# Optimization experiments

Hardware: AMD Instinct MI355X
Metric: run time of the kernel (lower is better)

The kernel has to match this reference:

```python
import jax, jax.numpy as jnp
import numpy as np
from jax import lax

B, CIN, H, W = 8, 256, 32, 32
DK, DV, NH = 256, 256, 8
DKH = DK // NH
COUT = 512  # output_dim; conv path has COUT - DV channels
KS, PAD = 3, 1


def setup_inputs() -> dict:
    key = jax.random.key(0)
    ks = jax.random.split(key, 9)
    scale = DKH ** (-0.5)
    return {
        "x": jax.random.normal(ks[0], (B, CIN, H, W), jnp.float32),
        "w_qkv": jax.random.normal(ks[1], (2 * DK + DV, CIN), jnp.float32) * 0.02,
        "b_qkv": jnp.zeros((2 * DK + DV,), jnp.float32),
        "w_attn": jax.random.normal(ks[2], (DV, DV), jnp.float32) * 0.02,
        "b_attn": jnp.zeros((DV,), jnp.float32),
        "w_out": jax.random.normal(ks[3], (COUT - DV, CIN, KS, KS), jnp.float32) * 0.02,
        "b_out": jnp.zeros((COUT - DV,), jnp.float32),
        # original: dkh**-0.5 + torch.rand(2*W-1, dkh)
        "key_rel_w": scale + jax.random.uniform(ks[4], (2 * W - 1, DKH), jnp.float32),
        "key_rel_h": scale + jax.random.uniform(ks[5], (2 * H - 1, DKH), jnp.float32),
    }


def _conv1x1(x, w, b):
    return jnp.einsum("bchw,oc->bohw", x, w) + b[None, :, None, None]


def _rel_to_abs(x):
    # x: [b, nh, L, 2L-1] -> [b, nh, L, L] via pad-reshape-slice trick
    b, nh, L, _ = x.shape
    x = jnp.pad(x, ((0, 0), (0, 0), (0, 0), (0, 1)))            # [b,nh,L,2L]
    flat = x.reshape(b, nh, L * 2 * L)
    flat = jnp.pad(flat, ((0, 0), (0, 0), (0, L - 1)))
    final = flat.reshape(b, nh, L + 1, 2 * L - 1)
    return final[:, :, :L, L - 1:]


def _rel_logits_1d(q5, rel_k, h, w, nh, perm):
    # q5: [b, nh, dkh, h, w]; rel_k: [2w-1, dkh]
    b = q5.shape[0]
    rel = jnp.einsum("bhdxy,md->bhxym", q5, rel_k)               # [b,nh,h,w,2w-1]
    rel = rel.reshape(b, nh * h, w, 2 * w - 1)
    rel = _rel_to_abs(rel)                                        # [b,nh*h,w,w]
    rel = rel.reshape(b, nh, h, w, w)
    rel = jnp.broadcast_to(rel[:, :, :, None], (b, nh, h, h, w, w))
    rel = jnp.transpose(rel, perm)                                # [b,nh,H,W,H,W]
    return rel.reshape(b, nh, h * w, h * w)


def reference(x, w_qkv, b_qkv, w_attn, b_attn, w_out, b_out, key_rel_w, key_rel_h):
    b = x.shape[0]
    hw = H * W
    # parallel conv path (3x3, pad 1)
    conv_out = lax.conv_general_dilated(
        x, w_out, window_strides=(1, 1), padding=((PAD, PAD), (PAD, PAD)),
        dimension_numbers=("NCHW", "OIHW", "NCHW")) + b_out[None, :, None, None]
    # qkv via 1x1 conv
    qkv = _conv1x1(x, w_qkv, b_qkv)
    q, k, v = jnp.split(qkv, [DK, 2 * DK], axis=1)
    q = q.reshape(b, NH, DKH, hw) * (DKH ** (-0.5))
    k = k.reshape(b, NH, DKH, hw)
    v = v.reshape(b, NH, DV // NH, hw)
    logits = jnp.einsum("bhdq,bhdk->bhqk", q, k)                  # [b,nh,HW,HW]
    q5 = q.reshape(b, NH, DKH, H, W)
    w_rel = _rel_logits_1d(q5, key_rel_w, H, W, NH, (0, 1, 2, 4, 3, 5))
    h_rel = _rel_logits_1d(jnp.transpose(q5, (0, 1, 2, 4, 3)), key_rel_h, W, H, NH,
                           (0, 1, 4, 2, 5, 3))
    logits = logits + h_rel + w_rel
    weights = jax.nn.softmax(logits, axis=-1)
    attn = jnp.einsum("bhqk,bhdk->bhdq", weights, v)              # [b,nh,dvh,HW]
    attn = attn.reshape(b, DV, H, W)
    attn = _conv1x1(attn, w_attn, b_attn)
    return jnp.concatenate([conv_out, attn], axis=1)
```

## Files before the change

kernel.cpp:

```cpp
#include <hip/hip_runtime.h>
#include <hip/hip_bf16.h>


typedef __hip_bfloat16 bf16;
using short8 = __attribute__((ext_vector_type(8))) short;
using short4v = __attribute__((ext_vector_type(4))) short;
using f32x4 = __attribute__((ext_vector_type(4))) float;

__device__ __forceinline__ short f2bs(float f) {
  union { bf16 b; short s; } u; u.b = __float2bfloat16(f); return u.s;
}
__device__ __forceinline__ float bs2f(short s) {
  union { unsigned u; float f; } x; x.u = ((unsigned)(unsigned short)s) << 16;
  return x.f;
}

__global__ __launch_bounds__(256) void xpose(
    const float* __restrict__ X, short* __restrict__ xt,
    short* __restrict__ xb2) {
  const int b = blockIdx.x, r = blockIdx.y;
  const int tid = threadIdx.x;
  if (r == 0 || r == 33) {
    short8 z = {};
    short* dst = xt + (((size_t)b * 34 + r) * 34) * 256;
    for (int g = tid; g < 1088; g += 256) *(short8*)(dst + g * 8) = z;
    return;
  }
  __shared__ short xls[32][264];
  {
    const float* src = X + (size_t)b * 256 * 1024 + (r - 1) * 32;
    for (int it = 0; it < 8; ++it) {
      int idx = it * 256 + tid;
      int c = idx >> 3, pq = idx & 7;
      float4 f4 = *(const float4*)(src + (size_t)c * 1024 + pq * 4);
      xls[pq * 4 + 0][c] = f2bs(f4.x);
      xls[pq * 4 + 1][c] = f2bs(f4.y);
      xls[pq * 4 + 2][c] = f2bs(f4.z);
      xls[pq * 4 + 3][c] = f2bs(f4.w);
    }
  }
  __syncthreads();
  {
    short* dst = xt + (((size_t)b * 34 + r) * 34) * 256;
    for (int it = 0; it < 4; ++it) {
      int idx = it * 256 + tid;
      int cc = idx >> 5, co = idx & 31;
      short8 v = *(const short8*)&xls[cc][co * 8];
      *(short8*)(dst + (cc + 1) * 256 + co * 8) = v;
    }
    if (tid < 64) {
      short8 z = {};
      int cce = (tid >> 5) * 33, co = tid & 31;
      *(short8*)(dst + cce * 256 + co * 8) = z;
    }
  }
  {
    short* dst = xb2 + (((size_t)b * 64 + (r - 1) * 2) * 8) * 512;
    for (int it = 0; it < 4; ++it) {
      int g = it * 256 + tid;
      int half = g >> 9, c8 = (g >> 6) & 7, grp = (g >> 4) & 3, pcol = g & 15;
      short8 v = *(const short8*)&xls[half * 16 + pcol][c8 * 32 + grp * 8];
      *(short8*)(dst + ((half * 8 + c8) * 64 + grp * 16 + pcol) * 8) = v;
    }
  }
}

__global__ __launch_bounds__(256) void wpack(
    const float* __restrict__ Wc, short* __restrict__ Wb,
    const float* __restrict__ wq, short* __restrict__ Wq,
    const float* __restrict__ wa, short* __restrict__ Wa) {
  const int bid = blockIdx.x;
  const int tid = threadIdx.x;
  if (bid < 256) {
    __shared__ float ws[2304];
    const float* src = Wc + (size_t)bid * 2304;
    for (int it = 0; it < 9; ++it) ws[it * 256 + tid] = src[it * 256 + tid];
    __syncthreads();
#pragma unroll
    for (int tap = 0; tap < 9; ++tap)
      Wb[tap * 65536 + bid * 256 + tid] = f2bs(ws[tid * 9 + tap]);
  } else if (bid < 1024) {
    int idx = (bid - 256) * 256 + tid;
    Wq[idx] = f2bs(wq[idx]);
  } else {
    int idx = (bid - 1024) * 256 + tid;
    Wa[idx] = f2bs(wa[idx]);
  }
}

__global__ __launch_bounds__(256) void qkv_mfma(
    const short* __restrict__ Wq, const short* __restrict__ xb2,
    const float* __restrict__ bias,
    short* __restrict__ qsb, short* __restrict__ ksb, short* __restrict__ vtb) {
  const int tid = threadIdx.x;
  const int w = tid >> 6, lane = tid & 63;
  const int col = lane & 15, grp = lane >> 4, g8 = grp * 8;
  const int b = blockIdx.z;
  const int p0 = blockIdx.x * 64;
  const int og = blockIdx.y * 128;
  const int ob = og + w * 16;

  const short* wa0 = Wq + (size_t)(ob + col) * 256 + g8;
  const short* wa1 = wa0 + (size_t)64 * 256;
  const short* xpb = xb2 + (((size_t)b * 64 + blockIdx.x * 4) * 8) * 512 + lane * 8;

  f32x4 acc[2][4] = {};
#pragma unroll
  for (int c8 = 0; c8 < 8; ++c8) {
    const int chb = c8 * 32;
    short8 a0 = *(const short8*)(wa0 + chb);
    short8 a1 = *(const short8*)(wa1 + chb);
    short8 b0 = *(const short8*)(xpb + c8 * 512);
    short8 b1 = *(const short8*)(xpb + 4096 + c8 * 512);
    short8 b2 = *(const short8*)(xpb + 8192 + c8 * 512);
    short8 b3 = *(const short8*)(xpb + 12288 + c8 * 512);
    acc[0][0] = __builtin_amdgcn_mfma_f32_16x16x32_bf16(a0, b0, acc[0][0], 0, 0, 0);
    acc[0][1] = __builtin_amdgcn_mfma_f32_16x16x32_bf16(a0, b1, acc[0][1], 0, 0, 0);
    acc[0][2] = __builtin_amdgcn_mfma_f32_16x16x32_bf16(a0, b2, acc[0][2], 0, 0, 0);
    acc[0][3] = __builtin_amdgcn_mfma_f32_16x16x32_bf16(a0, b3, acc[0][3], 0, 0, 0);
    acc[1][0] = __builtin_amdgcn_mfma_f32_16x16x32_bf16(a1, b0, acc[1][0], 0, 0, 0);
    acc[1][1] = __builtin_amdgcn_mfma_f32_16x16x32_bf16(a1, b1, acc[1][1], 0, 0, 0);
    acc[1][2] = __builtin_amdgcn_mfma_f32_16x16x32_bf16(a1, b2, acc[1][2], 0, 0, 0);
    acc[1][3] = __builtin_amdgcn_mfma_f32_16x16x32_bf16(a1, b3, acc[1][3], 0, 0, 0);
  }

  const float qscale = 0.17677669529663687f;
#pragma unroll
  for (int j = 0; j < 2; ++j) {
    const int obase = ob + j * 64 + grp * 4;
    const int sect = obase >> 8;
    const int nh = (obase >> 5) & 7;
    const int d0 = obase & 31;
    const size_t hb = ((size_t)(b * 8 + nh)) * 1024;
    float bv[4];
#pragma unroll
    for (int r = 0; r < 4; ++r) bv[r] = bias[obase + r];
    if (sect == 0) {
#pragma unroll
      for (int pp = 0; pp < 4; ++pp) {
        const int p = p0 + pp * 16 + col;
        short4v o4;
#pragma unroll
        for (int r = 0; r < 4; ++r)
          o4[r] = f2bs((acc[j][pp][r] + bv[r]) * qscale);
        *(short4v*)&qsb[(hb + p) * 32 + d0] = o4;
      }
    } else if (sect == 1) {
#pragma unroll
      for (int pp = 0; pp < 4; ++pp) {
        const int p = p0 + pp * 16 + col;
        short4v o4;
#pragma unroll
        for (int r = 0; r < 4; ++r)
          o4[r] = f2bs(acc[j][pp][r] + bv[r]);
        *(short4v*)&ksb[(hb + p) * 32 + d0] = o4;
      }
    } else {
#pragma unroll
      for (int pp = 0; pp < 4; ++pp) {
        const int p = p0 + pp * 16 + col;
#pragma unroll
        for (int r = 0; r < 4; ++r)
          vtb[hb * 32 + (size_t)(d0 + r) * 1024 + p] = f2bs(acc[j][pp][r] + bv[r]);
      }
    }
  }
}

__global__ __launch_bounds__(256, 4) void attn_mfma(
    const short* __restrict__ qsb, const short* __restrict__ ksb,
    const short* __restrict__ vtb,
    const float* __restrict__ relw_g, const float* __restrict__ relh_g,
    short* __restrict__ amt) {
  const int tid = threadIdx.x;
  const int w = tid >> 6, lane = tid & 63;
  const int col = lane & 15, grp = lane >> 4, g8 = grp * 8;
  const int qt = blockIdx.x * 4 + w;
  const int bnh = blockIdx.y;
  const int q0 = qt * 16;
  const int i = qt >> 1;
  const int j0 = (qt & 1) * 16;

  const short* Qb = qsb + (size_t)bnh * 32768;
  const short* Kb = ksb + (size_t)bnh * 32768;
  const short* Vb = vtb + (size_t)bnh * 32768;

  __shared__ short Gh_s[4][16][68];
  __shared__ short kvb[2][8][512];
  __shared__ short Pt_s[4][2][16][40];
  short* Gw_w = &Pt_s[w][0][0][0];

  const short* gK = Kb + (size_t)(w * 16 + col) * 32 + g8;
  const short* gV = Vb + (size_t)((w & 1) * 16 + col) * 1024 + (w >> 1) * 32 + g8;

  short8 stgK = *(const short8*)gK;
  short8 stgV = *(const short8*)gV;

  short8 b_q = *(const short8*)(Qb + (q0 + col) * 32 + g8);

  {
    const float* rels[2] = {relh_g, relw_g};
#pragma unroll
    for (int tb = 0; tb < 2; ++tb) {
      const float* relg = rels[tb];
#pragma unroll
      for (int t = 0; t < 4; ++t) {
        int m = 16 * t + col;
        int mc = m > 62 ? 62 : m;
        const float* rp = relg + mc * 32 + g8;
        float4 f0 = *(const float4*)rp;
        float4 f1 = *(const float4*)(rp + 4);
        short8 ar;
        ar[0] = f2bs(f0.x); ar[1] = f2bs(f0.y);
        ar[2] = f2bs(f0.z); ar[3] = f2bs(f0.w);
        ar[4] = f2bs(f1.x); ar[5] = f2bs(f1.y);
        ar[6] = f2bs(f1.z); ar[7] = f2bs(f1.w);
        f32x4 d = __builtin_amdgcn_mfma_f32_16x16x32_bf16(
            ar, b_q, (f32x4){0.f, 0.f, 0.f, 0.f}, 0, 0, 0);
        short4v o;
        o[0] = f2bs(d[0]); o[1] = f2bs(d[1]);
        o[2] = f2bs(d[2]); o[3] = f2bs(d[3]);
        short* Gd = tb ? Gw_w : &Gh_s[w][0][0];
        *(short4v*)(Gd + col * 68 + 16 * t + grp * 4) = o;
      }
    }
  }
  __asm__ volatile("s_waitcnt lgkmcnt(0)" ::: "memory");

  float gw[8];
#pragma unroll
  for (int t = 0; t < 2; ++t)
#pragma unroll
    for (int r = 0; r < 4; ++r)
      gw[t * 4 + r] =
          bs2f(Gw_w[col * 68 + t * 16 + grp * 4 + r - j0 - col + 31]);

  const short8 a_one = {0x3F80, 0x3F80, 0x3F80, 0x3F80,
                        0x3F80, 0x3F80, 0x3F80, 0x3F80};

  f32x4 acc0 = {0.f, 0.f, 0.f, 0.f};
  f32x4 acc1 = {0.f, 0.f, 0.f, 0.f};
  f32x4 accl = {0.f, 0.f, 0.f, 0.f};

  short8 cvA0p = {}, cvA1p = {}, cvB0p = {}, cvB1p = {};

  *(short8*)&kvb[0][w][lane * 8] = stgK;
  *(short8*)&kvb[0][4 + w][lane * 8] = stgV;
  __syncthreads();

#pragma unroll 2
  for (int it = 0; it < 16; ++it) {
    const int cur = it & 1;
    if (it < 15) {
      stgK = *(const short8*)(gK + (size_t)(it + 1) * 2048);
      stgV = *(const short8*)(gV + (size_t)(it + 1) * 64);
    }
    short8 ck0  = *(const short8*)&kvb[cur][0][lane * 8];
    short8 ck1  = *(const short8*)&kvb[cur][1][lane * 8];
    short8 ck2  = *(const short8*)&kvb[cur][2][lane * 8];
    short8 ck3  = *(const short8*)&kvb[cur][3][lane * 8];
    short8 cva0 = *(const short8*)&kvb[cur][4][lane * 8];
    short8 cva1 = *(const short8*)&kvb[cur][5][lane * 8];
    short8 cvb0 = *(const short8*)&kvb[cur][6][lane * 8];
    short8 cvb1 = *(const short8*)&kvb[cur][7][lane * 8];

    f32x4 s0 = __builtin_amdgcn_mfma_f32_16x16x32_bf16(
        ck0, b_q, (f32x4){0.f, 0.f, 0.f, 0.f}, 0, 0, 0);
    f32x4 s1 = __builtin_amdgcn_mfma_f32_16x16x32_bf16(
        ck1, b_q, (f32x4){0.f, 0.f, 0.f, 0.f}, 0, 0, 0);
    f32x4 s2 = __builtin_amdgcn_mfma_f32_16x16x32_bf16(
        ck2, b_q, (f32x4){0.f, 0.f, 0.f, 0.f}, 0, 0, 0);
    f32x4 s3 = __builtin_amdgcn_mfma_f32_16x16x32_bf16(
        ck3, b_q, (f32x4){0.f, 0.f, 0.f, 0.f}, 0, 0, 0);

    if (it > 0) {
      short8 pA = *(const short8*)&Pt_s[w][0][col][g8];
      short8 pB = *(const short8*)&Pt_s[w][1][col][g8];
      acc0 = __builtin_amdgcn_mfma_f32_16x16x32_bf16(cvA0p, pA, acc0, 0, 0, 0);
      acc0 = __builtin_amdgcn_mfma_f32_16x16x32_bf16(cvB0p, pB, acc0, 0, 0, 0);
      acc1 = __builtin_amdgcn_mfma_f32_16x16x32_bf16(cvA1p, pA, acc1, 0, 0, 0);
      acc1 = __builtin_amdgcn_mfma_f32_16x16x32_bf16(cvB1p, pB, acc1, 0, 0, 0);
      accl = __builtin_amdgcn_mfma_f32_16x16x32_bf16(a_one, pA, accl, 0, 0, 0);
      accl = __builtin_amdgcn_mfma_f32_16x16x32_bf16(a_one, pB, accl, 0, 0, 0);
    }

    float ghA = bs2f(Gh_s[w][col][2 * it - i + 31]);
    float ghB = bs2f(Gh_s[w][col][2 * it + 1 - i + 31]);
    short4v p0, p1, p2, p3;
#pragma unroll
    for (int r = 0; r < 4; ++r) p0[r] = f2bs(__expf(s0[r] + ghA + gw[r]));
#pragma unroll
    for (int r = 0; r < 4; ++r) p1[r] = f2bs(__expf(s1[r] + ghA + gw[4 + r]));
#pragma unroll
    for (int r = 0; r < 4; ++r) p2[r] = f2bs(__expf(s2[r] + ghB + gw[r]));
#pragma unroll
    for (int r = 0; r < 4; ++r) p3[r] = f2bs(__expf(s3[r] + ghB + gw[4 + r]));
    *(short4v*)&Pt_s[w][0][col][grp * 4] = p0;
    *(short4v*)&Pt_s[w][0][col][16 + grp * 4] = p1;
    *(short4v*)&Pt_s[w][1][col][grp * 4] = p2;
    *(short4v*)&Pt_s[w][1][col][16 + grp * 4] = p3;

    if (it < 15) {
      *(short8*)&kvb[cur ^ 1][w][lane * 8] = stgK;
      *(short8*)&kvb[cur ^ 1][4 + w][lane * 8] = stgV;
    }
    cvA0p = cva0; cvA1p = cva1; cvB0p = cvb0; cvB1p = cvb1;
    __syncthreads();
  }

  {
    short8 pA = *(const short8*)&Pt_s[w][0][col][g8];
    short8 pB = *(const short8*)&Pt_s[w][1][col][g8];
    acc0 = __builtin_amdgcn_mfma_f32_16x16x32_bf16(cvA0p, pA, acc0, 0, 0, 0);
    acc0 = __builtin_amdgcn_mfma_f32_16x16x32_bf16(cvB0p, pB, acc0, 0, 0, 0);
    acc1 = __builtin_amdgcn_mfma_f32_16x16x32_bf16(cvA1p, pA, acc1, 0, 0, 0);
    acc1 = __builtin_amdgcn_mfma_f32_16x16x32_bf16(cvB1p, pB, acc1, 0, 0, 0);
    accl = __builtin_amdgcn_mfma_f32_16x16x32_bf16(a_one, pA, accl, 0, 0, 0);
    accl = __builtin_amdgcn_mfma_f32_16x16x32_bf16(a_one, pB, accl, 0, 0, 0);
  }

  float rn = 1.0f / accl[0];
  const int bq = bnh >> 3, nh = bnh & 7;
  short* amb = amt + ((size_t)bq * 1024 + q0 + col) * 256 + nh * 32;
  short4v o4a, o4b;
#pragma unroll
  for (int r = 0; r < 4; ++r) {
    o4a[r] = f2bs(acc0[r] * rn);
    o4b[r] = f2bs(acc1[r] * rn);
  }
  *(short4v*)&amb[grp * 4] = o4a;
  *(short4v*)&amb[16 + grp * 4] = o4b;
}

__global__ __launch_bounds__(256) void proj_mfma(
    const short* __restrict__ Wa, const short* __restrict__ amt,
    const float* __restrict__ bias, float* __restrict__ out) {
  const int tid = threadIdx.x;
  const int w = tid >> 6, lane = tid & 63;
  const int col = lane & 15, grp = lane >> 4, g8 = grp * 8;
  const int b = blockIdx.z;
  const int p0 = blockIdx.x * 64;
  const int og = blockIdx.y * 128;
  const int ob = og + w * 16;

  const short* wa0 = Wa + (size_t)(ob + col) * 256 + g8;
  const short* wa1 = wa0 + (size_t)64 * 256;
  const short* xp0 = amt + ((size_t)b * 1024 + p0 + col) * 256 + g8;
  const short* xp1 = xp0 + (size_t)16 * 256;
  const short* xp2 = xp0 + (size_t)32 * 256;
  const short* xp3 = xp0 + (size_t)48 * 256;

  f32x4 acc[2][4] = {};
#pragma unroll
  for (int c8 = 0; c8 < 8; ++c8) {
    const int chb = c8 * 32;
    short8 a0 = *(const short8*)(wa0 + chb);
    short8 a1 = *(const short8*)(wa1 + chb);
    short8 b0 = *(const short8*)(xp0 + chb);
    short8 b1 = *(const short8*)(xp1 + chb);
    short8 b2 = *(const short8*)(xp2 + chb);
    short8 b3 = *(const short8*)(xp3 + chb);
    acc[0][0] = __builtin_amdgcn_mfma_f32_16x16x32_bf16(a0, b0, acc[0][0], 0, 0, 0);
    acc[0][1] = __builtin_amdgcn_mfma_f32_16x16x32_bf16(a0, b1, acc[0][1], 0, 0, 0);
    acc[0][2] = __builtin_amdgcn_mfma_f32_16x16x32_bf16(a0, b2, acc[0][2], 0, 0, 0);
    acc[0][3] = __builtin_amdgcn_mfma_f32_16x16x32_bf16(a0, b3, acc[0][3], 0, 0, 0);
    acc[1][0] = __builtin_amdgcn_mfma_f32_16x16x32_bf16(a1, b0, acc[1][0], 0, 0, 0);
    acc[1][1] = __builtin_amdgcn_mfma_f32_16x16x32_bf16(a1, b1, acc[1][1], 0, 0, 0);
    acc[1][2] = __builtin_amdgcn_mfma_f32_16x16x32_bf16(a1, b2, acc[1][2], 0, 0, 0);
    acc[1][3] = __builtin_amdgcn_mfma_f32_16x16x32_bf16(a1, b3, acc[1][3], 0, 0, 0);
  }

#pragma unroll
  for (int j = 0; j < 2; ++j) {
    const int obase = ob + j * 64 + grp * 4;
    float bv[4];
#pragma unroll
    for (int r = 0; r < 4; ++r) bv[r] = bias[obase + r];
#pragma unroll
    for (int pp = 0; pp < 4; ++pp) {
      const int p = p0 + pp * 16 + col;
#pragma unroll
      for (int r = 0; r < 4; ++r)
        out[((size_t)b * 512 + 256 + obase + r) * 1024 + p] =
            acc[j][pp][r] + bv[r];
    }
  }
}

__global__ __launch_bounds__(256) void conv_mfma(
    const short* __restrict__ xt, const short* __restrict__ Wb,
    const float* __restrict__ bias, float* __restrict__ out) {
  const int tid = threadIdx.x;
  const int w = tid >> 6, lane = tid & 63;
  const int col = lane & 15, grp = lane >> 4, g8 = grp * 8;
  const int r0 = blockIdx.x;
  const int oh = blockIdx.y;
  const int bb = blockIdx.z;

  __shared__ short xs[3][34][264];

  {
    const short* src = xt + (((size_t)bb * 34 + r0) * 34) * 256;
    for (int g = tid; g < 3264; g += 256) {
      int row = g / 1088;
      int rem = g - row * 1088;
      int cc = rem >> 5, chg = rem & 31;
      short8 v = *(const short8*)(src + (row * 34 + cc) * 256 + chg * 8);
      *(short8*)&xs[row][cc][chg * 8] = v;
    }
  }
  __syncthreads();

  const int ob0 = oh * 128 + w * 16;
  const int ob1 = ob0 + 64;
  const short* Wa0 = Wb + (ob0 + col) * 256 + g8;
  const short* Wa1 = Wb + (ob1 + col) * 256 + g8;

  f32x4 acc00 = {0.f, 0.f, 0.f, 0.f};
  f32x4 acc01 = {0.f, 0.f, 0.f, 0.f};
  f32x4 acc10 = {0.f, 0.f, 0.f, 0.f};
  f32x4 acc11 = {0.f, 0.f, 0.f, 0.f};

#pragma unroll 1
  for (int tap = 0; tap < 9; ++tap) {
    const int u = (tap * 11) >> 5, v = tap - 3 * u;
    const short* wa0 = Wa0 + tap * 65536;
    const short* wa1 = Wa1 + tap * 65536;
    const short* xb0 = &xs[u][col + v][g8];
    const short* xb1 = &xs[u][col + 16 + v][g8];
#pragma unroll
    for (int c8 = 0; c8 < 8; ++c8) {
      const int chb = c8 * 32;
      short8 a0 = *(const short8*)(wa0 + chb);
      short8 a1 = *(const short8*)(wa1 + chb);
      short8 b0 = *(const short8*)(xb0 + chb);
      short8 b1 = *(const short8*)(xb1 + chb);
      acc00 = __builtin_amdgcn_mfma_f32_16x16x32_bf16(a0, b0, acc00, 0, 0, 0);
      acc01 = __builtin_amdgcn_mfma_f32_16x16x32_bf16(a0, b1, acc01, 0, 0, 0);
      acc10 = __builtin_amdgcn_mfma_f32_16x16x32_bf16(a1, b0, acc10, 0, 0, 0);
      acc11 = __builtin_amdgcn_mfma_f32_16x16x32_bf16(a1, b1, acc11, 0, 0, 0);
    }
  }

  float* ob = out + (size_t)bb * 512 * 1024 + r0 * 32;
#pragma unroll
  for (int r = 0; r < 4; ++r) {
    int o0 = ob0 + grp * 4 + r;
    int o1 = ob1 + grp * 4 + r;
    float bv0 = bias[o0], bv1 = bias[o1];
    ob[(size_t)o0 * 1024 + col]      = acc00[r] + bv0;
    ob[(size_t)o0 * 1024 + 16 + col] = acc01[r] + bv0;
    ob[(size_t)o1 * 1024 + col]      = acc10[r] + bv1;
    ob[(size_t)o1 * 1024 + 16 + col] = acc11[r] + bv1;
  }
}

extern "C" void kernel_launch(void* const* d_in, const int* in_sizes, int n_in,
                              void* d_out, int out_size, void* d_ws, size_t ws_size,
                              hipStream_t stream) {
  const float* x      = (const float*)d_in[0];
  const float* w_qkv  = (const float*)d_in[1];
  const float* b_qkv  = (const float*)d_in[2];
  const float* w_attn = (const float*)d_in[3];
  const float* b_attn = (const float*)d_in[4];
  const float* w_out  = (const float*)d_in[5];
  const float* b_out  = (const float*)d_in[6];
  const float* relw   = (const float*)d_in[7];
  const float* relh   = (const float*)d_in[8];
  float* out = (float*)d_out;

  short* qsb = (short*)d_ws;
  short* ksb = qsb + (size_t)2 * 1024 * 1024;
  short* vtb = ksb + (size_t)2 * 1024 * 1024;
  short* amt = (short*)((char*)d_ws + (size_t)12 * 1024 * 1024);
  short* xt  = (short*)((char*)d_ws + (size_t)16 * 1024 * 1024);
  short* xb2 = (short*)((char*)d_ws + (size_t)21 * 1024 * 1024);
  short* Wq  = (short*)((char*)d_ws + (size_t)25 * 1024 * 1024);
  short* Wa  = (short*)((char*)d_ws + (size_t)25 * 1024 * 1024 + 512 * 1024);
  short* Wb  = (short*)((char*)d_ws + (size_t)26 * 1024 * 1024);

  xpose<<<dim3(8, 34), 256, 0, stream>>>(x, xt, xb2);
  wpack<<<1280, 256, 0, stream>>>(w_out, Wb, w_qkv, Wq, w_attn, Wa);
  qkv_mfma<<<dim3(16, 6, 8), 256, 0, stream>>>(Wq, xb2, b_qkv, qsb, ksb, vtb);
  attn_mfma<<<dim3(16, 64), 256, 0, stream>>>(qsb, ksb, vtb, relw, relh, amt);
  proj_mfma<<<dim3(16, 2, 8), 256, 0, stream>>>(Wa, amt, b_attn, out);
  conv_mfma<<<dim3(32, 2, 8), 256, 0, stream>>>(xt, Wb, b_out, out);
}
```

Measured before the change: 169.9 us.

## Pre-tile weights and K/V/attn buffers into MFMA fragment order for coalesced loads

Weights for qkv, projection and conv are packed into a 16x32 tile layout matching the MFMA operand fragment, so each lane reads a contiguous 16-byte chunk and a wave reads 1 KB. K, V and the attention output are written by producers in the same fragment-tiled order, so the attention and projection kernels load them as fully contiguous per-wave blocks. This targets strided, poorly coalesced global loads, at the cost of more scattered stores in the producer epilogues, especially the per-element V stores.

New measurement: 151.9 us. 1.12x faster.

```diff
diff --git a/kernel.cpp b/kernel.cpp
--- a/kernel.cpp
+++ b/kernel.cpp
@@ -13,6 +13,11 @@
 __device__ __forceinline__ float bs2f(short s) {
   union { unsigned u; float f; } x; x.u = ((unsigned)(unsigned short)s) << 16;
   return x.f;
+}
+
+__device__ __forceinline__ size_t wtile(int o, int c) {
+  return ((size_t)((o >> 4) * 8 + (c >> 5)) * 512) +
+         (((c >> 3) & 3) * 16 + (o & 15)) * 8 + (c & 7);
 }
 
 __global__ __launch_bounds__(256) void xpose(
@@ -66,9 +71,9 @@
 }
 
 __global__ __launch_bounds__(256) void wpack(
-    const float* __restrict__ Wc, short* __restrict__ Wb,
-    const float* __restrict__ wq, short* __restrict__ Wq,
-    const float* __restrict__ wa, short* __restrict__ Wa) {
+    const float* __restrict__ Wc, short* __restrict__ Wb2,
+    const float* __restrict__ wq, short* __restrict__ Wq2,
+    const float* __restrict__ wa, short* __restrict__ Wa2) {
   const int bid = blockIdx.x;
   const int tid = threadIdx.x;
   if (bid < 256) {
@@ -76,40 +81,40 @@
     const float* src = Wc + (size_t)bid * 2304;
     for (int it = 0; it < 9; ++it) ws[it * 256 + tid] = src[it * 256 + tid];
     __syncthreads();
+    const int o = bid, c = tid;
 #pragma unroll
     for (int tap = 0; tap < 9; ++tap)
-      Wb[tap * 65536 + bid * 256 + tid] = f2bs(ws[tid * 9 + tap]);
+      Wb2[(size_t)tap * 65536 + wtile(o, c)] = f2bs(ws[c * 9 + tap]);
   } else if (bid < 1024) {
-    int idx = (bid - 256) * 256 + tid;
-    Wq[idx] = f2bs(wq[idx]);
+    const int o = bid - 256, c = tid;
+    Wq2[wtile(o, c)] = f2bs(wq[o * 256 + c]);
   } else {
-    int idx = (bid - 1024) * 256 + tid;
-    Wa[idx] = f2bs(wa[idx]);
+    const int o = bid - 1024, c = tid;
+    Wa2[wtile(o, c)] = f2bs(wa[o * 256 + c]);
   }
 }
 
 __global__ __launch_bounds__(256) void qkv_mfma(
-    const short* __restrict__ Wq, const short* __restrict__ xb2,
+    const short* __restrict__ Wq2, const short* __restrict__ xb2,
     const float* __restrict__ bias,
-    short* __restrict__ qsb, short* __restrict__ ksb, short* __restrict__ vtb) {
+    short* __restrict__ qsb, short* __restrict__ ksb2, short* __restrict__ vtb2) {
   const int tid = threadIdx.x;
   const int w = tid >> 6, lane = tid & 63;
-  const int col = lane & 15, grp = lane >> 4, g8 = grp * 8;
+  const int col = lane & 15, grp = lane >> 4;
   const int b = blockIdx.z;
-  const int p0 = blockIdx.x * 64;
-  const int og = blockIdx.y * 128;
-  const int ob = og + w * 16;
-
-  const short* wa0 = Wq + (size_t)(ob + col) * 256 + g8;
-  const short* wa1 = wa0 + (size_t)64 * 256;
-  const short* xpb = xb2 + (((size_t)b * 64 + blockIdx.x * 4) * 8) * 512 + lane * 8;
+  const int bx = blockIdx.x;
+  const int p0 = bx * 64;
+  const int ob = blockIdx.y * 128 + w * 16;
+  const int o16 = ob >> 4;
+
+  const short* wbase = Wq2 + lane * 8;
+  const short* xpb = xb2 + (((size_t)b * 64 + bx * 4) * 8) * 512 + lane * 8;
 
   f32x4 acc[2][4] = {};
 #pragma unroll
   for (int c8 = 0; c8 < 8; ++c8) {
-    const int chb = c8 * 32;
-    short8 a0 = *(const short8*)(wa0 + chb);
-    short8 a1 = *(const short8*)(wa1 + chb);
+    short8 a0 = *(const short8*)(wbase + (size_t)(o16 * 8 + c8) * 512);
+    short8 a1 = *(const short8*)(wbase + (size_t)((o16 + 4) * 8 + c8) * 512);
     short8 b0 = *(const short8*)(xpb + c8 * 512);
     short8 b1 = *(const short8*)(xpb + 4096 + c8 * 512);
     short8 b2 = *(const short8*)(xpb + 8192 + c8 * 512);
@@ -132,6 +137,7 @@
     const int nh = (obase >> 5) & 7;
     const int d0 = obase & 31;
     const size_t hb = ((size_t)(b * 8 + nh)) * 1024;
+    const size_t hb2 = ((size_t)(b * 8 + nh)) * 32768;
     float bv[4];
 #pragma unroll
     for (int r = 0; r < 4; ++r) bv[r] = bias[obase + r];
@@ -146,32 +152,35 @@
         *(short4v*)&qsb[(hb + p) * 32 + d0] = o4;
       }
     } else if (sect == 1) {
+      const size_t kb = hb2 + (size_t)bx * 2048 + (w & 1) * 256 +
+                        (grp >> 1) * 128 + col * 8 + (grp & 1) * 4;
 #pragma unroll
       for (int pp = 0; pp < 4; ++pp) {
-        const int p = p0 + pp * 16 + col;
         short4v o4;
 #pragma unroll
         for (int r = 0; r < 4; ++r)
           o4[r] = f2bs(acc[j][pp][r] + bv[r]);
-        *(short4v*)&ksb[(hb + p) * 32 + d0] = o4;
+        *(short4v*)&ksb2[kb + pp * 512] = o4;
       }
     } else {
+      const size_t vb0 = hb2 + (size_t)bx * 2048 + (size_t)(w & 1) * 512 +
+                         (col >> 3) * 128 + (grp * 4) * 8 + (col & 7);
 #pragma unroll
       for (int pp = 0; pp < 4; ++pp) {
-        const int p = p0 + pp * 16 + col;
+        const size_t vb = vb0 + (pp >> 1) * 1024 + (pp & 1) * 256;
 #pragma unroll
         for (int r = 0; r < 4; ++r)
-          vtb[hb * 32 + (size_t)(d0 + r) * 1024 + p] = f2bs(acc[j][pp][r] + bv[r]);
+          vtb2[vb + r * 8] = f2bs(acc[j][pp][r] + bv[r]);
       }
     }
   }
 }
 
 __global__ __launch_bounds__(256, 4) void attn_mfma(
-    const short* __restrict__ qsb, const short* __restrict__ ksb,
-    const short* __restrict__ vtb,
+    const short* __restrict__ qsb, const short* __restrict__ ksb2,
+    const short* __restrict__ vtb2,
     const float* __restrict__ relw_g, const float* __restrict__ relh_g,
-    short* __restrict__ amt) {
+    short* __restrict__ amt2) {
   const int tid = threadIdx.x;
   const int w = tid >> 6, lane = tid & 63;
   const int col = lane & 15, grp = lane >> 4, g8 = grp * 8;
@@ -182,16 +191,14 @@
   const int j0 = (qt & 1) * 16;
 
   const short* Qb = qsb + (size_t)bnh * 32768;
-  const short* Kb = ksb + (size_t)bnh * 32768;
-  const short* Vb = vtb + (size_t)bnh * 32768;
 
   __shared__ short Gh_s[4][16][68];
   __shared__ short kvb[2][8][512];
   __shared__ short Pt_s[4][2][16][40];
   short* Gw_w = &Pt_s[w][0][0][0];
 
-  const short* gK = Kb + (size_t)(w * 16 + col) * 32 + g8;
-  const short* gV = Vb + (size_t)((w & 1) * 16 + col) * 1024 + (w >> 1) * 32 + g8;
+  const short* gK = ksb2 + (size_t)bnh * 32768 + w * 512 + lane * 8;
+  const short* gV = vtb2 + (size_t)bnh * 32768 + w * 512 + lane * 8;
 
   short8 stgK = *(const short8*)gK;
   short8 stgV = *(const short8*)gV;
@@ -253,7 +260,7 @@
     const int cur = it & 1;
     if (it < 15) {
       stgK = *(const short8*)(gK + (size_t)(it + 1) * 2048);
-      stgV = *(const short8*)(gV + (size_t)(it + 1) * 64);
+      stgV = *(const short8*)(gV + (size_t)(it + 1) * 2048);
     }
     short8 ck0  = *(const short8*)&kvb[cur][0][lane * 8];
     short8 ck1  = *(const short8*)&kvb[cur][1][lane * 8];
@@ -321,45 +328,42 @@
 
   float rn = 1.0f / accl[0];
   const int bq = bnh >> 3, nh = bnh & 7;
-  short* amb = amt + ((size_t)bq * 1024 + q0 + col) * 256 + nh * 32;
+  short* amb = amt2 + (((size_t)bq * 64 + qt) * 8 + nh) * 512 +
+               (grp >> 1) * 128 + col * 8 + (grp & 1) * 4;
   short4v o4a, o4b;
 #pragma unroll
   for (int r = 0; r < 4; ++r) {
     o4a[r] = f2bs(acc0[r] * rn);
     o4b[r] = f2bs(acc1[r] * rn);
   }
-  *(short4v*)&amb[grp * 4] = o4a;
-  *(short4v*)&amb[16 + grp * 4] = o4b;
+  *(short4v*)&amb[0] = o4a;
+  *(short4v*)&amb[256] = o4b;
 }
 
 __global__ __launch_bounds__(256) void proj_mfma(
-    const short* __restrict__ Wa, const short* __restrict__ amt,
+    const short* __restrict__ Wa2, const short* __restrict__ amt2,
     const float* __restrict__ bias, float* __restrict__ out) {
   const int tid = threadIdx.x;
   const int w = tid >> 6, lane = tid & 63;
-  const int col = lane & 15, grp = lane >> 4, g8 = grp * 8;
+  const int col = lane & 15, grp = lane >> 4;
   const int b = blockIdx.z;
-  const int p0 = blockIdx.x * 64;
-  const int og = blockIdx.y * 128;
-  const int ob = og + w * 16;
-
-  const short* wa0 = Wa + (size_t)(ob + col) * 256 + g8;
-  const short* wa1 = wa0 + (size_t)64 * 256;
-  const short* xp0 = amt + ((size_t)b * 1024 + p0 + col) * 256 + g8;
-  const short* xp1 = xp0 + (size_t)16 * 256;
-  const short* xp2 = xp0 + (size_t)32 * 256;
-  const short* xp3 = xp0 + (size_t)48 * 256;
+  const int bx = blockIdx.x;
+  const int p0 = bx * 64;
+  const int ob = blockIdx.y * 128 + w * 16;
+  const int o16 = ob >> 4;
+
+  const short* wbase = Wa2 + lane * 8;
+  const short* xpb = amt2 + (((size_t)b * 64 + bx * 4) * 8) * 512 + lane * 8;
 
   f32x4 acc[2][4] = {};
 #pragma unroll
   for (int c8 = 0; c8 < 8; ++c8) {
-    const int chb = c8 * 32;
-    short8 a0 = *(const short8*)(wa0 + chb);
-    short8 a1 = *(const short8*)(wa1 + chb);
-    short8 b0 = *(const short8*)(xp0 + chb);
-    short8 b1 = *(const short8*)(xp1 + chb);
-    short8 b2 = *(const short8*)(xp2 + chb);
-    short8 b3 = *(const short8*)(xp3 + chb);
+    short8 a0 = *(const short8*)(wbase + (size_t)(o16 * 8 + c8) * 512);
+    short8 a1 = *(const short8*)(wbase + (size_t)((o16 + 4) * 8 + c8) * 512);
+    short8 b0 = *(const short8*)(xpb + c8 * 512);
+    short8 b1 = *(const short8*)(xpb + 4096 + c8 * 512);
+    short8 b2 = *(const short8*)(xpb + 8192 + c8 * 512);
+    short8 b3 = *(const short8*)(xpb + 12288 + c8 * 512);
     acc[0][0] = __builtin_amdgcn_mfma_f32_16x16x32_bf16(a0, b0, acc[0][0], 0, 0, 0);
     acc[0][1] = __builtin_amdgcn_mfma_f32_16x16x32_bf16(a0, b1, acc[0][1], 0, 0, 0);
     acc[0][2] = __builtin_amdgcn_mfma_f32_16x16x32_bf16(a0, b2, acc[0][2], 0, 0, 0);
@@ -388,7 +392,7 @@
 }
 
 __global__ __launch_bounds__(256) void conv_mfma(
-    const short* __restrict__ xt, const short* __restrict__ Wb,
+    const short* __restrict__ xt, const short* __restrict__ Wb2,
     const float* __restrict__ bias, float* __restrict__ out) {
   const int tid = threadIdx.x;
   const int w = tid >> 6, lane = tid & 63;
@@ -412,9 +416,8 @@
   __syncthreads();
 
   const int ob0 = oh * 128 + w * 16;
-  const int ob1 = ob0 + 64;
-  const short* Wa0 = Wb + (ob0 + col) * 256 + g8;
-  const short* Wa1 = Wb + (ob1 + col) * 256 + g8;
+  const int o16_0 = oh * 8 + w;
+  const short* wbase = Wb2 + lane * 8;
 
   f32x4 acc00 = {0.f, 0.f, 0.f, 0.f};
   f32x4 acc01 = {0.f, 0.f, 0.f, 0.f};
@@ -424,15 +427,14 @@
 #pragma unroll 1
   for (int tap = 0; tap < 9; ++tap) {
     const int u = (tap * 11) >> 5, v = tap - 3 * u;
-    const short* wa0 = Wa0 + tap * 65536;
-    const short* wa1 = Wa1 + tap * 65536;
+    const short* wt = wbase + (size_t)tap * 65536;
     const short* xb0 = &xs[u][col + v][g8];
     const short* xb1 = &xs[u][col + 16 + v][g8];
 #pragma unroll
     for (int c8 = 0; c8 < 8; ++c8) {
       const int chb = c8 * 32;
-      short8 a0 = *(const short8*)(wa0 + chb);
-      short8 a1 = *(const short8*)(wa1 + chb);
+      short8 a0 = *(const short8*)(wt + (size_t)(o16_0 * 8 + c8) * 512);
+      short8 a1 = *(const short8*)(wt + (size_t)((o16_0 + 4) * 8 + c8) * 512);
       short8 b0 = *(const short8*)(xb0 + chb);
       short8 b1 = *(const short8*)(xb1 + chb);
       acc00 = __builtin_amdgcn_mfma_f32_16x16x32_bf16(a0, b0, acc00, 0, 0, 0);
@@ -442,6 +444,7 @@
     }
   }
 
+  const int ob1 = ob0 + 64;
   float* ob = out + (size_t)bb * 512 * 1024 + r0 * 32;
 #pragma unroll
   for (int r = 0; r < 4; ++r) {
@@ -469,20 +472,20 @@
   const float* relh   = (const float*)d_in[8];
   float* out = (float*)d_out;
 
-  short* qsb = (short*)d_ws;
-  short* ksb = qsb + (size_t)2 * 1024 * 1024;
-  short* vtb = ksb + (size_t)2 * 1024 * 1024;
-  short* amt = (short*)((char*)d_ws + (size_t)12 * 1024 * 1024);
-  short* xt  = (short*)((char*)d_ws + (size_t)16 * 1024 * 1024);
-  short* xb2 = (short*)((char*)d_ws + (size_t)21 * 1024 * 1024);
-  short* Wq  = (short*)((char*)d_ws + (size_t)25 * 1024 * 1024);
-  short* Wa  = (short*)((char*)d_ws + (size_t)25 * 1024 * 1024 + 512 * 1024);
-  short* Wb  = (short*)((char*)d_ws + (size_t)26 * 1024 * 1024);
+  short* qsb  = (short*)d_ws;
+  short* ksb2 = qsb + (size_t)2 * 1024 * 1024;
+  short* vtb2 = ksb2 + (size_t)2 * 1024 * 1024;
+  short* amt2 = (short*)((char*)d_ws + (size_t)12 * 1024 * 1024);
+  short* xt   = (short*)((char*)d_ws + (size_t)16 * 1024 * 1024);
+  short* xb2  = (short*)((char*)d_ws + (size_t)21 * 1024 * 1024);
+  short* Wq2  = (short*)((char*)d_ws + (size_t)25 * 1024 * 1024);
+  short* Wa2  = (short*)((char*)d_ws + (size_t)25 * 1024 * 1024 + 512 * 1024);
+  short* Wb2  = (short*)((char*)d_ws + (size_t)26 * 1024 * 1024);
 
   xpose<<<dim3(8, 34), 256, 0, stream>>>(x, xt, xb2);
-  wpack<<<1280, 256, 0, stream>>>(w_out, Wb, w_qkv, Wq, w_attn, Wa);
-  qkv_mfma<<<dim3(16, 6, 8), 256, 0, stream>>>(Wq, xb2, b_qkv, qsb, ksb, vtb);
-  attn_mfma<<<dim3(16, 64), 256, 0, stream>>>(qsb, ksb, vtb, relw, relh, amt);
-  proj_mfma<<<dim3(16, 2, 8), 256, 0, stream>>>(Wa, amt, b_attn, out);
-  conv_mfma<<<dim3(32, 2, 8), 256, 0, stream>>>(xt, Wb, b_out, out);
-}
+  wpack<<<1280, 256, 0, stream>>>(w_out, Wb2, w_qkv, Wq2, w_attn, Wa2);
+  qkv_mfma<<<dim3(16, 6, 8), 256, 0, stream>>>(Wq2, xb2, b_qkv, qsb, ksb2, vtb2);
+  attn_mfma<<<dim3(16, 64), 256, 0, stream>>>(qsb, ksb2, vtb2, relw, relh, amt2);
+  proj_mfma<<<dim3(16, 2, 8), 256, 0, stream>>>(Wa2, amt2, b_attn, out);
+  conv_mfma<<<dim3(32, 2, 8), 256, 0, stream>>>(xt, Wb2, b_out, out);
+}
```
